# Performance work log

Hardware: AMD Instinct MI355X
Metric: run time of the kernel (lower is better)

Reference implementation:

```python
import math
import jax, jax.numpy as jnp
import numpy as np

B, C, H, W = 16, 512, 32, 32
NUM_HEADS = 4
GROUPS = 32
EPS = 1e-5


def setup_inputs() -> dict:
    key = jax.random.key(0)
    ks = jax.random.split(key, 3)
    x = jax.random.normal(ks[0], (B, C, H, W), dtype=jnp.float32)
    # conv weights: kaiming-ish scale for 1x1 convs (fan_in = C)
    qkv_w = jax.random.normal(ks[1], (3 * C, C), dtype=jnp.float32) * (1.0 / math.sqrt(C))
    proj_w = jax.random.normal(ks[2], (C, C), dtype=jnp.float32) * (1.0 / math.sqrt(C))
    return {
        "x": x,
        "norm_w": jnp.ones((C,), jnp.float32),
        "norm_b": jnp.zeros((C,), jnp.float32),
        "qkv_w": qkv_w,
        "qkv_b": jnp.zeros((3 * C,), jnp.float32),
        "proj_w": proj_w,
        "proj_b": jnp.zeros((C,), jnp.float32),
    }


def group_norm(x, w, b):
    bN, c, h, wd = x.shape
    xg = x.reshape(bN, GROUPS, c // GROUPS, h, wd)
    mean = xg.mean(axis=(2, 3, 4), keepdims=True)
    var = xg.var(axis=(2, 3, 4), keepdims=True)
    xg = (xg - mean) * jax.lax.rsqrt(var + EPS)
    x = xg.reshape(bN, c, h, wd)
    return x * w[None, :, None, None] + b[None, :, None, None]


def conv1x1(x, w, b):
    # x: (b,c,h,w), w: (out,in), b: (out,)
    return jnp.einsum('bchw,oc->bohw', x, w) + b[None, :, None, None]


def reference(x, norm_w, norm_b, qkv_w, qkv_b, proj_w, proj_b):
    b, c, h, w = x.shape
    hd = c // NUM_HEADS  # head dim
    n = h * w            # tokens
    qkv = conv1x1(group_norm(x, norm_w, norm_b), qkv_w, qkv_b)
    q, k, v = jnp.split(qkv, 3, axis=1)
    # (b, heads, hd, n)
    q = q.reshape(b, NUM_HEADS, hd, n)
    k = k.reshape(b, NUM_HEADS, hd, n)
    v = v.reshape(b, NUM_HEADS, hd, n)
    # attn: (b, heads, n, n)
    attn = jnp.einsum('bhdn,bhdm->bhnm', q, k) / math.sqrt(hd)
    attn = jax.nn.softmax(attn, axis=-1)
    # out: (b, heads, n, hd) -> (b, c, h, w)
    out = jnp.einsum('bhnm,bhdm->bhnd', attn, v)
    out = out.transpose(0, 1, 3, 2).reshape(b, c, h, w)
    return x + conv1x1(out, proj_w, proj_b)
```

## Files before the change

kernel.cpp:

```cpp
#include <hip/hip_runtime.h>
#include <stdint.h>

#define DEV __device__ __forceinline__

typedef __attribute__((ext_vector_type(4))) float f32x4;
typedef __attribute__((ext_vector_type(8))) short s16x8;
typedef __attribute__((ext_vector_type(8))) __bf16 bf16x8;

constexpr int kB = 16, kC = 512, kN = 1024;
constexpr int kO = 1536;
constexpr int kG = 32, kCPG = 16;
constexpr float kEps = 1e-5f;
constexpr float kQS = 0.08838834764831845f * 1.44269504088896f;

#if __has_builtin(__builtin_amdgcn_exp2f)
#define EXP2(x) __builtin_amdgcn_exp2f(x)
#else
#define EXP2(x) exp2f(x)
#endif

DEV unsigned short f2bf(float f) {
  union { float f; uint32_t u; } cv; cv.f = f;
  uint32_t u = cv.u;
  return (unsigned short)((u + 0x7FFFu + ((u >> 16) & 1u)) >> 16);
}

DEV unsigned short bfbits(float f) {
  __bf16 h = (__bf16)f;
  return __builtin_bit_cast(unsigned short, h);
}

DEV bf16x8 asbf(s16x8 v) { return __builtin_bit_cast(bf16x8, v); }

DEV void gl_lds16(const void* g, void* l) {
  __builtin_amdgcn_global_load_lds(
      (const __attribute__((address_space(1))) uint32_t*)g,
      (__attribute__((address_space(3))) uint32_t*)l, 16, 0, 0);
}

__global__ __launch_bounds__(256) void k_wconv2(const float* __restrict__ qw,
                                                const float* __restrict__ pw,
                                                unsigned short* __restrict__ dq,
                                                unsigned short* __restrict__ dp) {
  const int nq = 1536 * 512 / 4, np = 512 * 512 / 4;
  int i = blockIdx.x * 256 + threadIdx.x;
  const float* src;
  unsigned short* dst;
  int j;
  if (i < nq) { src = qw; dst = dq; j = i; }
  else { j = i - nq; if (j >= np) return; src = pw; dst = dp; }
  f32x4 v = ((const f32x4*)src)[j];
  unsigned short o[4];
  o[0] = f2bf(v[0]); o[1] = f2bf(v[1]); o[2] = f2bf(v[2]); o[3] = f2bf(v[3]);
  ((uint2*)dst)[j] = *(uint2*)o;
}

__global__ __launch_bounds__(256) void k_gnstats(const float* __restrict__ x,
                                                 float* __restrict__ meanp,
                                                 float* __restrict__ rstdp) {
  int bg = blockIdx.x;
  const f32x4* p4 = (const f32x4*)(x + (size_t)bg * (kCPG * kN));
  float s = 0.f, s2 = 0.f;
  for (int i = threadIdx.x; i < (kCPG * kN / 4); i += 256) {
    f32x4 v = p4[i];
    s += v[0] + v[1] + v[2] + v[3];
    s2 += v[0] * v[0] + v[1] * v[1] + v[2] * v[2] + v[3] * v[3];
  }
#pragma unroll
  for (int m = 32; m >= 1; m >>= 1) { s += __shfl_xor(s, m); s2 += __shfl_xor(s2, m); }
  __shared__ float rb[8];
  int lane = threadIdx.x & 63, wid = threadIdx.x >> 6;
  if (lane == 0) { rb[wid * 2] = s; rb[wid * 2 + 1] = s2; }
  __syncthreads();
  if (threadIdx.x == 0) {
    float S = rb[0] + rb[2] + rb[4] + rb[6];
    float S2 = rb[1] + rb[3] + rb[5] + rb[7];
    float mu = S * (1.f / 16384.f);
    float var = S2 * (1.f / 16384.f) - mu * mu;
    meanp[bg] = mu;
    rstdp[bg] = rsqrtf(var + kEps);
  }
}

__global__ __launch_bounds__(256) void k_gnapply(const float* __restrict__ x,
                                                 const float* __restrict__ gw,
                                                 const float* __restrict__ gb,
                                                 const float* __restrict__ meanp,
                                                 const float* __restrict__ rstdp,
                                                 unsigned short* __restrict__ xt) {
  int bid = blockIdx.x;
  int b = bid >> 7;
  int ct = (bid >> 4) & 7;
  int nt = bid & 15;
  int c0 = ct * 64, n0 = nt * 64;
  __shared__ float tile[64][65];
  int t = threadIdx.x;
#pragma unroll
  for (int pass = 0; pass < 4; ++pass) {
    int r = pass * 16 + (t >> 4);
    int col = (t & 15) << 2;
    int c = c0 + r;
    f32x4 v = *(const f32x4*)(x + ((size_t)b * kC + c) * kN + n0 + col);
    int g = b * kG + (c >> 4);
    float rs = rstdp[g];
    float a = rs * gw[c];
    float bb = gb[c] - meanp[g] * a;
    tile[r][col + 0] = v[0] * a + bb;
    tile[r][col + 1] = v[1] * a + bb;
    tile[r][col + 2] = v[2] * a + bb;
    tile[r][col + 3] = v[3] * a + bb;
  }
  __syncthreads();
#pragma unroll
  for (int pass = 0; pass < 2; ++pass) {
    int nr = pass * 32 + (t >> 3);
    int cb = (t & 7) << 3;
    unsigned short o[8];
#pragma unroll
    for (int j = 0; j < 8; ++j) o[j] = f2bf(tile[cb + j][nr]);
    *(uint4*)(xt + ((size_t)b * kN + n0 + nr) * kC + c0 + cb) = *(uint4*)o;
  }
}

template <int MODE>
__global__ __launch_bounds__(256, 2) void k_gemm(const unsigned short* __restrict__ act,
                                                 const unsigned short* __restrict__ wb,
                                                 const float* __restrict__ bias,
                                                 unsigned short* __restrict__ qkT,
                                                 unsigned short* __restrict__ vbuf,
                                                 const float* __restrict__ xres,
                                                 float* __restrict__ outp) {
  int b = blockIdx.y;
  int nt = blockIdx.x & 7, ot = blockIdx.x >> 3;
  int n0 = nt << 7, o0 = ot << 7;
  int t = threadIdx.x, lane = t & 63, wid = t >> 6;
  int wr = wid >> 1, wc = wid & 1;
  __shared__ unsigned short sA[2][128 * 64];
  __shared__ unsigned short sB[2][128 * 64];
  f32x4 acc[4][4];
  const f32x4 zf = {0.f, 0.f, 0.f, 0.f};
#pragma unroll
  for (int i = 0; i < 4; ++i)
#pragma unroll
    for (int j = 0; j < 4; ++j) acc[i][j] = zf;
  const size_t rowb = (size_t)b * kN;

  auto stage = [&](int buf, int kt) {
    const int k0 = kt << 6;
#pragma unroll
    for (int p = 0; p < 4; ++p) {
      const int id = p * 256 + t;
      const int row = id >> 3, cp = id & 7;
      const int cl = cp ^ (row & 7);
      gl_lds16(act + (rowb + n0 + row) * (size_t)kC + k0 + cl * 8,
               (char*)sA[buf] + (p * 256 + wid * 64) * 16);
      gl_lds16(wb + (size_t)(o0 + row) * kC + k0 + cl * 8,
               (char*)sB[buf] + (p * 256 + wid * 64) * 16);
    }
  };

  stage(0, 0);
#pragma unroll 1
  for (int kt = 0; kt < 8; ++kt) {
    const int cur = kt & 1;
    asm volatile("s_waitcnt vmcnt(0)" ::: "memory");
    __syncthreads();
    if (kt < 7) stage(cur ^ 1, kt + 1);
    __builtin_amdgcn_s_setprio(1);
#pragma unroll
    for (int kk = 0; kk < 2; ++kk) {
      s16x8 af[4], bfr[4];
      const int cl = kk * 4 + (lane >> 4);
#pragma unroll
      for (int i = 0; i < 4; ++i) {
        const int rA = wr * 64 + i * 16 + (lane & 15);
        af[i] = *(const s16x8*)((const char*)sA[cur] + rA * 128 + ((cl ^ (rA & 7)) << 4));
        const int rB = wc * 64 + i * 16 + (lane & 15);
        bfr[i] = *(const s16x8*)((const char*)sB[cur] + rB * 128 + ((cl ^ (rB & 7)) << 4));
      }
#pragma unroll
      for (int i = 0; i < 4; ++i)
#pragma unroll
        for (int j = 0; j < 4; ++j)
          acc[i][j] = __builtin_amdgcn_mfma_f32_16x16x32_bf16(asbf(af[i]), asbf(bfr[j]),
                                                              acc[i][j], 0, 0, 0);
    }
    __builtin_amdgcn_s_setprio(0);
  }
  const int baseN = n0 + wr * 64 + ((lane >> 4) << 2);
#pragma unroll
  for (int j = 0; j < 4; ++j) {
    const int o = o0 + wc * 64 + j * 16 + (lane & 15);
    const float bs = bias[o];
#pragma unroll
    for (int i = 0; i < 4; ++i) {
      const int nb = baseN + i * 16;
      if (MODE == 0) {
        if (o < 1024) {
          const float sc = (o < 512) ? kQS : 1.0f;
#pragma unroll
          for (int r = 0; r < 4; ++r)
            qkT[(rowb + nb + r) * (size_t)kO + o] = f2bf((acc[i][j][r] + bs) * sc);
        } else {
          unsigned short pk[4];
#pragma unroll
          for (int r = 0; r < 4; ++r) pk[r] = f2bf(acc[i][j][r] + bs);
          *(uint2*)(vbuf + ((size_t)b * 512 + (o - 1024)) * kN + nb) = *(uint2*)pk;
        }
      } else {
        const size_t oo = ((size_t)b * kC + o) * kN + nb;
        const f32x4 xv = *(const f32x4*)(xres + oo);
        f32x4 ov;
        ov[0] = acc[i][j][0] + bs + xv[0];
        ov[1] = acc[i][j][1] + bs + xv[1];
        ov[2] = acc[i][j][2] + bs + xv[2];
        ov[3] = acc[i][j][3] + bs + xv[3];
        *(f32x4*)(outp + oo) = ov;
      }
    }
  }
}

__global__ __launch_bounds__(256, 2) void k_attn(const unsigned short* __restrict__ qkT,
                                                 const unsigned short* __restrict__ vbuf,
                                                 unsigned short* __restrict__ aoT) {
  const int bh = blockIdx.x, qt = blockIdx.y;
  const int b = bh >> 2, h = bh & 3;
  const int t = threadIdx.x, lane = t & 63, wid = t >> 6;
  __shared__ unsigned short sK[2][64 * 128];
  __shared__ unsigned short sV[2][128 * 64];
  __shared__ unsigned short sP[128 * 64];
  const int qrow0 = qt * 128 + wid * 32;
  s16x8 qf[2][4];
#pragma unroll
  for (int bi = 0; bi < 2; ++bi)
#pragma unroll
    for (int kk = 0; kk < 4; ++kk)
      qf[bi][kk] = *(const s16x8*)(qkT + ((size_t)b * kN + qrow0 + bi * 16 + (lane & 15)) * kO +
                                   h * 128 + kk * 32 + ((lane >> 4) << 3));
  f32x4 oc[2][8];
  const f32x4 zf = {0.f, 0.f, 0.f, 0.f};
#pragma unroll
  for (int bi = 0; bi < 2; ++bi)
#pragma unroll
    for (int dj = 0; dj < 8; ++dj) oc[bi][dj] = zf;
  float lpart[8];
#pragma unroll
  for (int i = 0; i < 8; ++i) lpart[i] = 0.f;

  auto stage = [&](int buf, int m0) {
#pragma unroll
    for (int p = 0; p < 4; ++p) {
      const int id = p * 256 + t;
      {
        const int row = id >> 4, cp = id & 15, cl = cp ^ (row & 7);
        gl_lds16(qkT + ((size_t)b * kN + m0 + row) * kO + 512 + h * 128 + cl * 8,
                 (char*)sK[buf] + (p * 256 + wid * 64) * 16);
      }
      {
        const int row = id >> 3, cp = id & 7, cl = cp ^ (row & 7);
        gl_lds16(vbuf + ((size_t)b * 512 + h * 128 + row) * kN + m0 + cl * 8,
                 (char*)sV[buf] + (p * 256 + wid * 64) * 16);
      }
    }
  };

  stage(0, 0);
#pragma unroll 1
  for (int mt = 0; mt < 16; ++mt) {
    const int cur = mt & 1;
    asm volatile("s_waitcnt vmcnt(0)" ::: "memory");
    __syncthreads();
    if (mt < 15) stage(cur ^ 1, (mt + 1) * 64);
    f32x4 sacc[2][4];
#pragma unroll
    for (int bi = 0; bi < 2; ++bi)
#pragma unroll
      for (int j = 0; j < 4; ++j) sacc[bi][j] = zf;
    __builtin_amdgcn_s_setprio(1);
#pragma unroll
    for (int kk = 0; kk < 4; ++kk) {
      s16x8 kf[4];
      const int cl = kk * 4 + (lane >> 4);
#pragma unroll
      for (int j = 0; j < 4; ++j) {
        const int rm = j * 16 + (lane & 15);
        kf[j] = *(const s16x8*)((const char*)sK[cur] + rm * 256 + ((cl ^ (rm & 7)) << 4));
      }
#pragma unroll
      for (int bi = 0; bi < 2; ++bi)
#pragma unroll
        for (int j = 0; j < 4; ++j)
          sacc[bi][j] = __builtin_amdgcn_mfma_f32_16x16x32_bf16(asbf(qf[bi][kk]), asbf(kf[j]),
                                                                sacc[bi][j], 0, 0, 0);
    }
    __builtin_amdgcn_s_setprio(0);
#pragma unroll
    for (int bi = 0; bi < 2; ++bi)
#pragma unroll
      for (int r = 0; r < 4; ++r) {
        const int nrow = wid * 32 + bi * 16 + ((lane >> 4) << 2) + r;
        float pvs = 0.f;
#pragma unroll
        for (int j = 0; j < 4; ++j) {
          const float p = EXP2(sacc[bi][j][r]);
          pvs += p;
          const int m = j * 16 + (lane & 15);
          *(unsigned short*)((char*)sP + nrow * 128 + (((m >> 3) ^ (nrow & 7)) << 4) +
                             ((m & 7) << 1)) = bfbits(p);
        }
        lpart[bi * 4 + r] += pvs;
      }
    __builtin_amdgcn_s_setprio(1);
#pragma unroll
    for (int ks = 0; ks < 2; ++ks) {
      s16x8 pf[2], vf[8];
      const int cl = ks * 4 + (lane >> 4);
#pragma unroll
      for (int bi = 0; bi < 2; ++bi) {
        const int rp = wid * 32 + bi * 16 + (lane & 15);
        pf[bi] = *(const s16x8*)((const char*)sP + rp * 128 + ((cl ^ (rp & 7)) << 4));
      }
#pragma unroll
      for (int dj = 0; dj < 8; ++dj) {
        const int rv = dj * 16 + (lane & 15);
        vf[dj] = *(const s16x8*)((const char*)sV[cur] + rv * 128 + ((cl ^ (rv & 7)) << 4));
      }
#pragma unroll
      for (int bi = 0; bi < 2; ++bi)
#pragma unroll
        for (int dj = 0; dj < 8; ++dj)
          oc[bi][dj] = __builtin_amdgcn_mfma_f32_16x16x32_bf16(asbf(pf[bi]), asbf(vf[dj]),
                                                               oc[bi][dj], 0, 0, 0);
    }
    __builtin_amdgcn_s_setprio(0);
  }
#pragma unroll
  for (int bi = 0; bi < 2; ++bi) {
#pragma unroll
    for (int r = 0; r < 4; ++r) {
      float ls = lpart[bi * 4 + r];
#pragma unroll
      for (int st = 1; st <= 8; st <<= 1) ls += __shfl_xor(ls, st);
      const float inv = 1.f / ls;
      const int n = qrow0 + bi * 16 + ((lane >> 4) << 2) + r;
#pragma unroll
      for (int dj = 0; dj < 8; ++dj) {
        const int d = dj * 16 + (lane & 15);
        aoT[((size_t)b * kN + n) * kC + h * 128 + d] = bfbits(oc[bi][dj][r] * inv);
      }
    }
  }
}

extern "C" void kernel_launch(void* const* d_in, const int* in_sizes, int n_in,
                              void* d_out, int out_size, void* d_ws, size_t ws_size,
                              hipStream_t stream) {
  const float* x = (const float*)d_in[0];
  const float* norm_w = (const float*)d_in[1];
  const float* norm_b = (const float*)d_in[2];
  const float* qkv_w = (const float*)d_in[3];
  const float* qkv_b = (const float*)d_in[4];
  const float* proj_w = (const float*)d_in[5];
  const float* proj_b = (const float*)d_in[6];
  float* out = (float*)d_out;
  char* ws = (char*)d_ws;
  const size_t OFF_MEAN = 0;
  const size_t OFF_RSTD = 2048;
  const size_t OFF_WQ = 4096;
  const size_t OFF_WP = OFF_WQ + (size_t)1536 * 512 * 2;
  const size_t OFF_XT = OFF_WP + (size_t)512 * 512 * 2;
  const size_t OFF_QKT = OFF_XT + (size_t)16 * 1024 * 512 * 2;
  const size_t OFF_V = OFF_QKT + (size_t)16 * 1024 * 1536 * 2;
  const size_t NEED = OFF_V + (size_t)16 * 512 * 1024 * 2;
  if (ws_size < NEED) return;
  float* meanp = (float*)(ws + OFF_MEAN);
  float* rstdp = (float*)(ws + OFF_RSTD);
  unsigned short* wq = (unsigned short*)(ws + OFF_WQ);
  unsigned short* wp = (unsigned short*)(ws + OFF_WP);
  unsigned short* xt = (unsigned short*)(ws + OFF_XT);
  unsigned short* qkT = (unsigned short*)(ws + OFF_QKT);
  unsigned short* vb = (unsigned short*)(ws + OFF_V);
  unsigned short* aoT = xt;

  k_wconv2<<<1024, 256, 0, stream>>>(qkv_w, proj_w, wq, wp);
  k_gnstats<<<512, 256, 0, stream>>>(x, meanp, rstdp);
  k_gnapply<<<2048, 256, 0, stream>>>(x, norm_w, norm_b, meanp, rstdp, xt);
  k_gemm<0><<<dim3(96, 16), 256, 0, stream>>>(xt, wq, qkv_b, qkT, vb, nullptr, nullptr);
  k_attn<<<dim3(64, 8), 256, 0, stream>>>(qkT, vb, aoT);
  k_gemm<1><<<dim3(32, 16), 256, 0, stream>>>(aoT, wp, proj_b, nullptr, nullptr, x, out);
}
```

Baseline: 129.4 us.

## Triple-buffer GEMM with BK=32 stages and LDS-staged coalesced QK stores

The QKV/proj GEMM moves from a double-buffered BK=64 pipeline to a three-stage ring of BK=32 tiles. It waits with partial vmcnt so loads stay in flight across iterations, and raises launch bounds to 3 blocks per CU. The QK epilogue now transposes through LDS so stores to qkT are 16-byte coalesced rows rather than scattered 2-byte writes. The trade-offs are more barriers per K step, tighter register budget under 3-block occupancy, and extra LDS traffic in the epilogue.

Result: faster. 125.3 us (-3.2%).

```diff
diff --git a/kernel.cpp b/kernel.cpp
--- a/kernel.cpp
+++ b/kernel.cpp
@@ -123,7 +123,7 @@
 }
 
 template <int MODE>
-__global__ __launch_bounds__(256, 2) void k_gemm(const unsigned short* __restrict__ act,
+__global__ __launch_bounds__(256, 3) void k_gemm(const unsigned short* __restrict__ act,
                                                  const unsigned short* __restrict__ wb,
                                                  const float* __restrict__ bias,
                                                  unsigned short* __restrict__ qkT,
@@ -135,8 +135,7 @@
   int n0 = nt << 7, o0 = ot << 7;
   int t = threadIdx.x, lane = t & 63, wid = t >> 6;
   int wr = wid >> 1, wc = wid & 1;
-  __shared__ unsigned short sA[2][128 * 64];
-  __shared__ unsigned short sB[2][128 * 64];
+  __shared__ __align__(16) char smem[49152];
   f32x4 acc[4][4];
   const f32x4 zf = {0.f, 0.f, 0.f, 0.f};
 #pragma unroll
@@ -145,69 +144,104 @@
     for (int j = 0; j < 4; ++j) acc[i][j] = zf;
   const size_t rowb = (size_t)b * kN;
 
-  auto stage = [&](int buf, int kt) {
-    const int k0 = kt << 6;
-#pragma unroll
-    for (int p = 0; p < 4; ++p) {
+  auto stage = [&](int buf, int kt2) {
+    const int k0 = kt2 << 5;
+    char* dA = smem + buf * 8192;
+    char* dB = smem + 24576 + buf * 8192;
+#pragma unroll
+    for (int p = 0; p < 2; ++p) {
       const int id = p * 256 + t;
-      const int row = id >> 3, cp = id & 7;
-      const int cl = cp ^ (row & 7);
-      gl_lds16(act + (rowb + n0 + row) * (size_t)kC + k0 + cl * 8,
-               (char*)sA[buf] + (p * 256 + wid * 64) * 16);
-      gl_lds16(wb + (size_t)(o0 + row) * kC + k0 + cl * 8,
-               (char*)sB[buf] + (p * 256 + wid * 64) * 16);
+      const int row = id >> 2, cp = id & 3;
+      const int cl = cp ^ ((row >> 1) & 3);
+      gl_lds16(act + (rowb + n0 + row) * (size_t)kC + k0 + cl * 8, dA + id * 16);
+      gl_lds16(wb + (size_t)(o0 + row) * kC + k0 + cl * 8, dB + id * 16);
     }
   };
 
   stage(0, 0);
+  stage(1, 1);
+  int cur = 0, stg = 2;
 #pragma unroll 1
-  for (int kt = 0; kt < 8; ++kt) {
-    const int cur = kt & 1;
-    asm volatile("s_waitcnt vmcnt(0)" ::: "memory");
-    __syncthreads();
-    if (kt < 7) stage(cur ^ 1, kt + 1);
+  for (int kt = 0; kt < 16; ++kt) {
+    if (kt < 15) {
+      asm volatile("s_waitcnt vmcnt(4)" ::: "memory");
+    } else {
+      asm volatile("s_waitcnt vmcnt(0)" ::: "memory");
+    }
+    __builtin_amdgcn_s_barrier();
+    if (kt < 14) stage(stg, kt + 2);
+    const char* pA = smem + cur * 8192;
+    const char* pB = smem + 24576 + cur * 8192;
+    s16x8 af[4], bfr[4];
+    const int c = lane >> 4;
+#pragma unroll
+    for (int i = 0; i < 4; ++i) {
+      const int rA = wr * 64 + i * 16 + (lane & 15);
+      af[i] = *(const s16x8*)(pA + rA * 64 + ((c ^ ((rA >> 1) & 3)) << 4));
+      const int rB = wc * 64 + i * 16 + (lane & 15);
+      bfr[i] = *(const s16x8*)(pB + rB * 64 + ((c ^ ((rB >> 1) & 3)) << 4));
+    }
     __builtin_amdgcn_s_setprio(1);
 #pragma unroll
-    for (int kk = 0; kk < 2; ++kk) {
-      s16x8 af[4], bfr[4];
-      const int cl = kk * 4 + (lane >> 4);
-#pragma unroll
-      for (int i = 0; i < 4; ++i) {
-        const int rA = wr * 64 + i * 16 + (lane & 15);
-        af[i] = *(const s16x8*)((const char*)sA[cur] + rA * 128 + ((cl ^ (rA & 7)) << 4));
-        const int rB = wc * 64 + i * 16 + (lane & 15);
-        bfr[i] = *(const s16x8*)((const char*)sB[cur] + rB * 128 + ((cl ^ (rB & 7)) << 4));
-      }
-#pragma unroll
-      for (int i = 0; i < 4; ++i)
-#pragma unroll
-        for (int j = 0; j < 4; ++j)
-          acc[i][j] = __builtin_amdgcn_mfma_f32_16x16x32_bf16(asbf(af[i]), asbf(bfr[j]),
-                                                              acc[i][j], 0, 0, 0);
-    }
+    for (int i = 0; i < 4; ++i)
+#pragma unroll
+      for (int j = 0; j < 4; ++j)
+        acc[i][j] = __builtin_amdgcn_mfma_f32_16x16x32_bf16(asbf(af[i]), asbf(bfr[j]),
+                                                            acc[i][j], 0, 0, 0);
     __builtin_amdgcn_s_setprio(0);
-  }
-  const int baseN = n0 + wr * 64 + ((lane >> 4) << 2);
-#pragma unroll
-  for (int j = 0; j < 4; ++j) {
-    const int o = o0 + wc * 64 + j * 16 + (lane & 15);
-    const float bs = bias[o];
-#pragma unroll
-    for (int i = 0; i < 4; ++i) {
-      const int nb = baseN + i * 16;
-      if (MODE == 0) {
-        if (o < 1024) {
-          const float sc = (o < 512) ? kQS : 1.0f;
-#pragma unroll
-          for (int r = 0; r < 4; ++r)
-            qkT[(rowb + nb + r) * (size_t)kO + o] = f2bf((acc[i][j][r] + bs) * sc);
-        } else {
+    cur = (cur == 2) ? 0 : cur + 1;
+    stg = (stg == 2) ? 0 : stg + 1;
+  }
+
+  if (MODE == 0) {
+    if (o0 < 1024) {
+      __syncthreads();
+      const float sc = (o0 < 512) ? kQS : 1.0f;
+      unsigned short* tile = (unsigned short*)smem;
+#pragma unroll
+      for (int j = 0; j < 4; ++j) {
+        const int o = wc * 64 + j * 16 + (lane & 15);
+        const float bs = bias[o0 + o];
+#pragma unroll
+        for (int i = 0; i < 4; ++i)
+#pragma unroll
+          for (int r = 0; r < 4; ++r) {
+            const int n = wr * 64 + i * 16 + ((lane >> 4) << 2) + r;
+            tile[n * 136 + o] = f2bf((acc[i][j][r] + bs) * sc);
+          }
+      }
+      __syncthreads();
+#pragma unroll
+      for (int it = 0; it < 8; ++it) {
+        const int n = it * 16 + (t >> 4);
+        const int c8 = t & 15;
+        *(uint4*)(qkT + (rowb + n0 + n) * (size_t)kO + o0 + c8 * 8) =
+            *(const uint4*)(tile + n * 136 + c8 * 8);
+      }
+    } else {
+#pragma unroll
+      for (int j = 0; j < 4; ++j) {
+        const int o = o0 + wc * 64 + j * 16 + (lane & 15);
+        const float bs = bias[o];
+#pragma unroll
+        for (int i = 0; i < 4; ++i) {
+          const int nb = n0 + wr * 64 + ((lane >> 4) << 2) + i * 16;
           unsigned short pk[4];
 #pragma unroll
           for (int r = 0; r < 4; ++r) pk[r] = f2bf(acc[i][j][r] + bs);
           *(uint2*)(vbuf + ((size_t)b * 512 + (o - 1024)) * kN + nb) = *(uint2*)pk;
         }
-      } else {
+      }
+    }
+  } else {
+    const int baseN = n0 + wr * 64 + ((lane >> 4) << 2);
+#pragma unroll
+    for (int j = 0; j < 4; ++j) {
+      const int o = o0 + wc * 64 + j * 16 + (lane & 15);
+      const float bs = bias[o];
+#pragma unroll
+      for (int i = 0; i < 4; ++i) {
+        const int nb = baseN + i * 16;
         const size_t oo = ((size_t)b * kC + o) * kN + nb;
         const f32x4 xv = *(const f32x4*)(xres + oo);
         f32x4 ov;
```
